# Performance work log

Hardware: AMD Instinct MI355X
Metric: run time of the kernel (lower is better)

## Reference

```python
import jax, jax.numpy as jnp
import numpy as np

B = 48            # graph pairs
NQ, NC = 20, 16   # query / corpus node counts (corpus padded to NMAX)
NMAX = 20         # max_node_set_size
DN, DE = 16, 8    # raw node / edge feature dims
D = 32            # node_state_dim
EH = 64           # edge_hidden_sizes[-1]
EQ, EC = 80, 60   # edges per query / corpus graph
PROP = 5          # n_prop_layers
TEMP = 0.01       # sinkhorn temperature
ITERS = 20        # sinkhorn iterations
LAMBDA = 1.0
NTOT = B * (NQ + NC)
NE = B * (EQ + EC)
SRC, DST = np.triu_indices(NMAX, 1)   # nC2 = 190 node pairs
_indq = np.ones(NMAX, np.int32)
_indc = np.array([1] * NC + [0] * (NMAX - NC), np.int32)
NXOR = jnp.asarray((_indq[:, None] ^ _indc[None, :]).astype(np.float32))  # [20,20]


def _mlp2(x, w1, b1, w2, b2):
    return jnp.maximum(x @ w1 + b1, 0.0) @ w2 + b2


def _sinkhorn(log_alpha):
    la = log_alpha / TEMP
    for _ in range(ITERS):
        la = la - jax.nn.logsumexp(la, axis=2, keepdims=True)
        la = la - jax.nn.logsumexp(la, axis=1, keepdims=True)
    return jnp.exp(la)


def _edge_emb(H, adj, w1, b1, w2, b2):
    s, d = H[:, SRC], H[:, DST]            # [B,nC2,D] gathers
    e = adj[:, SRC, DST][..., None]        # [B,nC2,1]
    f = _mlp2(jnp.concatenate([s, d, e], -1), w1, b1, w2, b2)
    bk = _mlp2(jnp.concatenate([d, s, e], -1), w1, b1, w2, b2)
    return f + bk                          # bidirectional msg, [B,nC2,EH]


def _forward(node_features, edge_features, query_adj, corpus_adj,
             enc_nw, enc_nb, enc_ew, enc_eb,
             msg_w1, msg_b1, msg_w2, msg_b2,
             upd_w1, upd_b1, upd_w2, upd_b2,
             sink_w1, sink_b1, sink_w2, sink_b2,
             lrl_w1, lrl_b1, lrl_w2, lrl_b2,
             from_idx, to_idx):
    h = node_features @ enc_nw + enc_nb    # GMN encoder (linear MLPs)
    e = edge_features @ enc_ew + enc_eb
    for _ in range(PROP):                  # shared-param propagation
        msg = _mlp2(jnp.concatenate([h[from_idx], h[to_idx], e], -1),
                    msg_w1, msg_b1, msg_w2, msg_b2)
        agg = jax.ops.segment_sum(msg, to_idx, num_segments=NTOT)
        h = h + _mlp2(jnp.concatenate([agg, h], -1), upd_w1, upd_b1, upd_w2, upd_b2)
    hp = h.reshape(B, NQ + NC, D)          # split_and_stack (static sizes)
    Hq = hp[:, :NQ]
    Hc = jnp.pad(hp[:, NQ:], ((0, 0), (0, NMAX - NC), (0, 0)))
    tq = _mlp2(Hq, sink_w1, sink_b1, sink_w2, sink_b2)
    tc = _mlp2(Hc, sink_w1, sink_b1, sink_w2, sink_b2)
    cost = jnp.abs(tq[:, :, None, :] - tc[:, None, :, :]).sum(-1)  # cdist p=1
    P = _sinkhorn(-cost)                   # node transport plan [B,20,20]
    Eq = _edge_emb(Hq, query_adj, lrl_w1, lrl_b1, lrl_w2, lrl_b2)
    Ec = _edge_emb(Hc, corpus_adj, lrl_w1, lrl_b1, lrl_w2, lrl_b2)
    Pa, Pb = P[:, SRC, :], P[:, DST, :]
    straight = Pa[:, :, SRC] * Pb[:, :, DST]    # plan[src_i,src_j]*plan[dst_i,dst_j]
    cross = Pa[:, :, DST] * Pb[:, :, SRC]
    eT = straight + cross                  # use_max=False, no second sinkhorn
    aq = query_adj[:, SRC, DST].astype(jnp.int32)
    ac = corpus_adj[:, SRC, DST].astype(jnp.int32)
    pxor = (aq[:, :, None] ^ ac[:, None, :]).astype(P.dtype)
    ediff = Eq[:, :, None, :] - Ec[:, None, :, :]   # [B,nC2,nC2,EH]
    ecost = jnp.maximum(ediff, 0.0).sum(-1) + jnp.maximum(-ediff, 0.0).sum(-1)
    edge_align = (pxor * eT * ecost).sum((-1, -2))
    ndiff = Hq[:, :, None, :] - Hc[:, None, :, :]   # [B,20,20,D]
    ncost = jnp.maximum(ndiff, 0.0).sum(-1) + jnp.maximum(-ndiff, 0.0).sum(-1)
    node_align = (NXOR * P * ncost).sum((-1, -2))
    return edge_align + LAMBDA * node_align         # [B]


def setup_inputs():
    key = jax.random.key(0)
    rng = np.random.default_rng(0)
    base = (np.arange(B) * (NQ + NC))[:, None]
    fq = base + rng.integers(0, NQ, (B, EQ)); tq = base + rng.integers(0, NQ, (B, EQ))
    fc = base + NQ + rng.integers(0, NC, (B, EC)); tc = base + NQ + rng.integers(0, NC, (B, EC))
    from_idx = jnp.asarray(np.concatenate([fq, fc], 1).reshape(-1), jnp.int32)
    to_idx = jnp.asarray(np.concatenate([tq, tc], 1).reshape(-1), jnp.int32)
    qadj = rng.integers(0, 2, (B, NMAX, NMAX)).astype(np.float32)
    cadj = rng.integers(0, 2, (B, NMAX, NMAX)).astype(np.float32)
    cadj[:, NC:, :] = 0.0; cadj[:, :, NC:] = 0.0   # padded corpus nodes have no edges
    ks = iter(jax.random.split(key, 32))
    def w(shape, s=0.1):
        return jax.random.normal(next(ks), shape, jnp.float32) * s
    return {
        'node_features': w((NTOT, DN), 1.0),
        'edge_features': w((NE, DE), 1.0),
        'query_adj': jnp.asarray(qadj),
        'corpus_adj': jnp.asarray(cadj),
        'enc_nw': w((DN, D)), 'enc_nb': w((D,)),
        'enc_ew': w((DE, 16)), 'enc_eb': w((16,)),
        'msg_w1': w((2 * D + 16, EH)), 'msg_b1': w((EH,)),
        'msg_w2': w((EH, EH)), 'msg_b2': w((EH,)),
        'upd_w1': w((EH + D, EH)), 'upd_b1': w((EH,)),
        'upd_w2': w((EH, D)), 'upd_b2': w((D,)),
        'sink_w1': w((D, NMAX)), 'sink_b1': w((NMAX,)),
        'sink_w2': w((NMAX, NMAX)), 'sink_b2': w((NMAX,)),
        'lrl_w1': w((2 * D + 1, EH)), 'lrl_b1': w((EH,)),
        'lrl_w2': w((EH, EH)), 'lrl_b2': w((EH,)),
        'from_idx': from_idx, 'to_idx': to_idx,
        'graph_sizes': jnp.asarray(np.tile([NQ, NC], B), jnp.int32),
    }


def reference(node_features, edge_features, query_adj, corpus_adj,
              enc_nw, enc_nb, enc_ew, enc_eb,
              msg_w1, msg_b1, msg_w2, msg_b2,
              upd_w1, upd_b1, upd_w2, upd_b2,
              sink_w1, sink_b1, sink_w2, sink_b2,
              lrl_w1, lrl_b1, lrl_w2, lrl_b2,
              from_idx, to_idx, graph_sizes):
    return _forward(node_features, edge_features, query_adj, corpus_adj,
                    enc_nw, enc_nb, enc_ew, enc_eb,
                    msg_w1, msg_b1, msg_w2, msg_b2,
                    upd_w1, upd_b1, upd_w2, upd_b2,
                    sink_w1, sink_b1, sink_w2, sink_b2,
                    lrl_w1, lrl_b1, lrl_w2, lrl_b2,
                    from_idx, to_idx)
```

## Files before the change

kernel.cpp:

```cpp
#include <hip/hip_runtime.h>


constexpr int kB    = 48;
constexpr int kNM   = 20;
constexpr int kD    = 32;
constexpr int kNP   = 190;
constexpr int kNTOT = 1728;
constexpr int kIters = 20;
constexpr float kInvT = 100.0f;

__device__ __forceinline__ void pair_sd(int p, int& s, int& d) {
    int row = 0, rem = p;
    #pragma unroll
    for (int r = 0; r < 19; ++r) {
        int len = 19 - r;
        if (rem < len) { row = r; break; }
        rem -= len;
    }
    s = row; d = row + 1 + rem;
}

__device__ __forceinline__ float bc(float v, int k) {
    return __int_as_float(__builtin_amdgcn_readlane(__float_as_int(v), k));
}

__device__ __forceinline__ void lse20(float (&r)[20]) {
    float m01 = fmaxf(r[0], r[1]),  m23 = fmaxf(r[2], r[3]),
          m45 = fmaxf(r[4], r[5]),  m67 = fmaxf(r[6], r[7]),
          m89 = fmaxf(r[8], r[9]),  mab = fmaxf(r[10], r[11]),
          mcd = fmaxf(r[12], r[13]), mef = fmaxf(r[14], r[15]),
          mgh = fmaxf(r[16], r[17]), mij = fmaxf(r[18], r[19]);
    float n0 = fmaxf(m01, m23), n1 = fmaxf(m45, m67), n2 = fmaxf(m89, mab),
          n3 = fmaxf(mcd, mef), n4 = fmaxf(mgh, mij);
    float m = fmaxf(fmaxf(fmaxf(n0, n1), fmaxf(n2, n3)), n4);
    float e[20];
    #pragma unroll
    for (int k = 0; k < 20; ++k) e[k] = __expf(r[k] - m);
    float s01 = e[0] + e[1],  s23 = e[2] + e[3],  s45 = e[4] + e[5],
          s67 = e[6] + e[7],  s89 = e[8] + e[9],  sab = e[10] + e[11],
          scd = e[12] + e[13], sef = e[14] + e[15], sgh = e[16] + e[17],
          sij = e[18] + e[19];
    float t0 = s01 + s23, t1 = s45 + s67, t2 = s89 + sab,
          t3 = scd + sef, t4 = sgh + sij;
    float s = ((t0 + t1) + (t2 + t3)) + t4;
    float l = m + __logf(s);
    #pragma unroll
    for (int k = 0; k < 20; ++k) r[k] -= l;
}

__global__ void k_enc(const float* __restrict__ nf, const float* __restrict__ nw,
                      const float* __restrict__ nb, const float* __restrict__ ef,
                      const float* __restrict__ ew, const float* __restrict__ eb,
                      float* __restrict__ h, float* __restrict__ ee,
                      float* __restrict__ agg, float* __restrict__ out) {
    int tid = blockIdx.x * 256 + threadIdx.x;
    int stride = gridDim.x * 256;
    for (int i = tid; i < kNTOT * 32; i += stride) {
        int n = i >> 5, c = i & 31;
        float acc = nb[c];
        const float* row = nf + n * 16;
        #pragma unroll
        for (int k = 0; k < 16; ++k) acc = fmaf(row[k], nw[k * 32 + c], acc);
        h[i] = acc;
    }
    for (int i = tid; i < 6720 * 16; i += stride) {
        int n = i >> 4, c = i & 15;
        float acc = eb[c];
        const float* row = ef + n * 8;
        #pragma unroll
        for (int k = 0; k < 8; ++k) acc = fmaf(row[k], ew[k * 16 + c], acc);
        ee[i] = acc;
    }
    for (int i = tid; i < kNTOT * 64; i += stride) agg[i] = 0.f;
    if (tid < kB) out[tid] = 0.f;
}

__global__ void __launch_bounds__(256)
k_msg(const float* __restrict__ h, const float* __restrict__ ee,
      const int* __restrict__ fidx, const int* __restrict__ tidx,
      const float* __restrict__ w1, const float* __restrict__ b1,
      const float* __restrict__ w2, const float* __restrict__ b2,
      float* __restrict__ agg) {
    int w = threadIdx.x >> 6, lane = threadIdx.x & 63;
    int e0 = (blockIdx.x * 4 + w) * 2;
    int toj[2]; float xa[2], xb[2], acc[2], o[2];
    #pragma unroll
    for (int j = 0; j < 2; ++j) {
        int e = e0 + j;
        int fr = fidx[e]; toj[j] = tidx[e];
        xa[j] = h[(lane < 32 ? fr : toj[j]) * kD + (lane & 31)];
        xb[j] = ee[e * 16 + (lane & 15)];
        acc[j] = b1[lane];
    }
    #pragma unroll
    for (int k = 0; k < 64; ++k) {
        float w1k = w1[k * 64 + lane];
        #pragma unroll
        for (int j = 0; j < 2; ++j) acc[j] = fmaf(bc(xa[j], k), w1k, acc[j]);
    }
    #pragma unroll
    for (int k = 0; k < 16; ++k) {
        float w1k = w1[(64 + k) * 64 + lane];
        #pragma unroll
        for (int j = 0; j < 2; ++j) acc[j] = fmaf(bc(xb[j], k), w1k, acc[j]);
    }
    #pragma unroll
    for (int j = 0; j < 2; ++j) { acc[j] = fmaxf(acc[j], 0.f); o[j] = b2[lane]; }
    #pragma unroll
    for (int k = 0; k < 64; ++k) {
        float w2k = w2[k * 64 + lane];
        #pragma unroll
        for (int j = 0; j < 2; ++j) o[j] = fmaf(bc(acc[j], k), w2k, o[j]);
    }
    #pragma unroll
    for (int j = 0; j < 2; ++j) atomicAdd(&agg[toj[j] * 64 + lane], o[j]);
}

__global__ void __launch_bounds__(256)
k_upd(float* __restrict__ h, float* __restrict__ agg,
      const float* __restrict__ w1, const float* __restrict__ b1,
      const float* __restrict__ w2, const float* __restrict__ b2) {
    int w = threadIdx.x >> 6, lane = threadIdx.x & 63;
    int n0 = (blockIdx.x * 4 + w) * 2;
    float xa[2], xb[2], acc[2], o[2];
    #pragma unroll
    for (int j = 0; j < 2; ++j) {
        int n = n0 + j;
        xa[j] = agg[n * 64 + lane];
        agg[n * 64 + lane] = 0.f;
        xb[j] = h[n * kD + (lane & 31)];
        acc[j] = b1[lane];
    }
    #pragma unroll
    for (int k = 0; k < 64; ++k) {
        float w1k = w1[k * 64 + lane];
        #pragma unroll
        for (int j = 0; j < 2; ++j) acc[j] = fmaf(bc(xa[j], k), w1k, acc[j]);
    }
    #pragma unroll
    for (int k = 0; k < 32; ++k) {
        float w1k = w1[(64 + k) * 64 + lane];
        #pragma unroll
        for (int j = 0; j < 2; ++j) acc[j] = fmaf(bc(xb[j], k), w1k, acc[j]);
    }
    #pragma unroll
    for (int j = 0; j < 2; ++j) { acc[j] = fmaxf(acc[j], 0.f); o[j] = b2[lane & 31]; }
    #pragma unroll
    for (int k = 0; k < 64; ++k) {
        float w2k = w2[k * 32 + (lane & 31)];
        #pragma unroll
        for (int j = 0; j < 2; ++j) o[j] = fmaf(bc(acc[j], k), w2k, o[j]);
    }
    if (lane < 32) {
        #pragma unroll
        for (int j = 0; j < 2; ++j) h[(n0 + j) * kD + lane] += o[j];
    }
}

__global__ void k_sink_t(const float* __restrict__ h,
                         const float* __restrict__ w1, const float* __restrict__ b1,
                         const float* __restrict__ w2, const float* __restrict__ b2,
                         float* __restrict__ Hq, float* __restrict__ Hc,
                         float* __restrict__ tq, float* __restrict__ tc) {
    __shared__ float xs[4][32];
    __shared__ float hs[4][20];
    int w = threadIdx.x >> 6, lane = threadIdx.x & 63;
    int xcd = blockIdx.x & 7, slot = blockIdx.x >> 3;
    int b = xcd + 8 * (slot / 10);
    int task = (slot % 10) * 4 + w;
    int side = task >= 20;
    int i = task - side * 20;
    if (lane < 32) {
        float v;
        if (side == 0) v = h[(b * 36 + i) * kD + lane];
        else           v = (i < 16) ? h[(b * 36 + 20 + i) * kD + lane] : 0.f;
        (side ? Hc : Hq)[(b * kNM + i) * kD + lane] = v;
        xs[w][lane] = v;
    }
    __syncthreads();
    if (lane < kNM) {
        float acc = b1[lane];
        #pragma unroll
        for (int k = 0; k < kD; ++k) acc += xs[w][k] * w1[k * kNM + lane];
        hs[w][lane] = fmaxf(acc, 0.f);
    }
    __syncthreads();
    if (lane < kNM) {
        float o = b2[lane];
        #pragma unroll
        for (int k = 0; k < kNM; ++k) o += hs[w][k] * w2[k * kNM + lane];
        (side ? tc : tq)[(b * kNM + i) * kNM + lane] = o;
    }
}

__global__ void k_sinkhorn(const float* __restrict__ tq, const float* __restrict__ tc,
                           const float* __restrict__ Hq,
                           float* __restrict__ P, float* __restrict__ out) {
    __shared__ float tcS[400];
    __shared__ float tr[20 * 21];
    int b = blockIdx.x, lane = threadIdx.x;
    for (int i = lane; i < 400; i += 64) tcS[i] = tc[b * 400 + i];
    int i20 = lane < 20 ? lane : 0;
    float tqr[20];
    #pragma unroll
    for (int k = 0; k < 20; ++k) tqr[k] = tq[(b * 20 + i20) * 20 + k];
    __syncthreads();
    float r[20];
    #pragma unroll
    for (int j = 0; j < 20; ++j) {
        float c = 0.f;
        #pragma unroll
        for (int k = 0; k < 20; ++k) c += fabsf(tqr[k] - tcS[j * 20 + k]);
        r[j] = -c * kInvT;
    }
    for (int it = 0; it < kIters; ++it) {
        lse20(r);
        if (lane < 20) {
            #pragma unroll
            for (int j = 0; j < 20; ++j) tr[lane * 21 + j] = r[j];
        }
        __syncthreads();
        if (lane < 20) {
            #pragma unroll
            for (int i = 0; i < 20; ++i) r[i] = tr[i * 21 + lane];
        }
        __syncthreads();
        lse20(r);
        if (lane < 20) {
            #pragma unroll
            for (int i = 0; i < 20; ++i) tr[i * 21 + lane] = r[i];
        }
        __syncthreads();
        if (lane < 20) {
            #pragma unroll
            for (int j = 0; j < 20; ++j) r[j] = tr[lane * 21 + j];
        }
        __syncthreads();
    }
    float part = 0.f;
    if (lane < 20) {
        float pv[20];
        #pragma unroll
        for (int j = 0; j < 20; ++j) pv[j] = __expf(r[j]);
        float* Pb = P + b * 400 + lane * 20;
        #pragma unroll
        for (int j = 0; j < 20; ++j) Pb[j] = pv[j];
        float pr4 = (pv[16] + pv[17]) + (pv[18] + pv[19]);
        float l1 = 0.f;
        const float* hq = Hq + (b * 20 + lane) * 32;
        #pragma unroll
        for (int k = 0; k < 32; ++k) l1 += fabsf(hq[k]);
        part = pr4 * l1;
    }
    #pragma unroll
    for (int off = 32; off; off >>= 1) part += __shfl_down(part, off, 64);
    if (lane == 0) atomicAdd(&out[b], part);
}

__global__ void __launch_bounds__(256)
k_edge_emb(const float* __restrict__ Hq, const float* __restrict__ Hc,
           const float* __restrict__ qadj, const float* __restrict__ cadj,
           const float* __restrict__ w1, const float* __restrict__ b1,
           const float* __restrict__ w2, const float* __restrict__ b2,
           float* __restrict__ Eq, float* __restrict__ Ec) {
    int w = threadIdx.x >> 6, lane = threadIdx.x & 63;
    int xcd = blockIdx.x & 7, slot = blockIdx.x >> 3;
    int b = xcd + 8 * (slot / 24);
    int r = slot % 24;
    float xa[4], ev[4], af[4], ab[4];
    int sidej[4], pj[4];
    #pragma unroll
    for (int j = 0; j < 4; ++j) {
        int tloc = r * 16 + w * 4 + j;
        if (tloc >= 380) tloc = 379;
        sidej[j] = tloc / kNP; pj[j] = tloc % kNP;
        int s, d; pair_sd(pj[j], s, d);
        const float* H = sidej[j] ? Hc : Hq;
        xa[j] = (lane < 32) ? H[(b * kNM + s) * kD + lane]
                            : H[(b * kNM + d) * kD + (lane - 32)];
        ev[j] = (sidej[j] ? cadj : qadj)[b * 400 + s * 20 + d];
        float bb = b1[lane];
        af[j] = bb; ab[j] = bb;
    }
    #pragma unroll
    for (int k = 0; k < 64; ++k) {
        float w1k = w1[k * 64 + lane];
        #pragma unroll
        for (int j = 0; j < 4; ++j) {
            af[j] = fmaf(bc(xa[j], k),      w1k, af[j]);
            ab[j] = fmaf(bc(xa[j], k ^ 32), w1k, ab[j]);
        }
    }
    {
        float w1e = w1[64 * 64 + lane];
        #pragma unroll
        for (int j = 0; j < 4; ++j) {
            af[j] = fmaf(ev[j], w1e, af[j]);
            ab[j] = fmaf(ev[j], w1e, ab[j]);
        }
    }
    float hid[4], o[4];
    #pragma unroll
    for (int j = 0; j < 4; ++j) {
        hid[j] = fmaxf(af[j], 0.f) + fmaxf(ab[j], 0.f);
        o[j] = 2.f * b2[lane];
    }
    #pragma unroll
    for (int k = 0; k < 64; ++k) {
        float w2k = w2[k * 64 + lane];
        #pragma unroll
        for (int j = 0; j < 4; ++j) o[j] = fmaf(bc(hid[j], k), w2k, o[j]);
    }
    #pragma unroll
    for (int j = 0; j < 4; ++j)
        (sidej[j] ? Ec : Eq)[(b * kNP + pj[j]) * 64 + lane] = o[j];
}

#define EC_ALL(X) X(0) X(1) X(2) X(3) X(4) X(5) X(6) X(7) X(8) X(9) X(10) X(11) \
  X(12) X(13) X(14) X(15) X(16) X(17) X(18) X(19) X(20) X(21) X(22) X(23) \
  X(24) X(25) X(26) X(27) X(28) X(29) X(30) X(31)

__global__ void __launch_bounds__(256, 4)
k_final(const float* __restrict__ P, const float* __restrict__ Eq,
        const float* __restrict__ Ec, const float* __restrict__ qadj,
        const float* __restrict__ cadj, float* __restrict__ out) {
    __shared__ float Ps[400];
    __shared__ unsigned char spsh[192], dpsh[192];
    int xcd = blockIdx.x & 7, slot = blockIdx.x >> 3;
    int b = xcd + 8 * (slot / 6), qt = slot % 6;
    int t = threadIdx.x, w = t >> 6, lane = t & 63;
    if (t < 192) {
        int s = 0, d = 0;
        if (t < kNP) pair_sd(t, s, d);
        spsh[t] = (unsigned char)s;
        dpsh[t] = (unsigned char)d;
    }
    for (int i = t; i < 400; i += 256) Ps[i] = P[b * 400 + i];
    __syncthreads();

    int l31 = lane & 31;
    int q = qt * 32 + l31;
    bool qv = q < kNP;
    int sq = spsh[qv ? q : 0], dq = dpsh[qv ? q : 0];
    float acv = qv ? cadj[b * 400 + sq * 20 + dq] : 0.f;

    const float* ecb = Ec + (b * kNP + qt * 32) * 64 + lane;
#define EC_DECL(i) float ec##i = (qt * 32 + i < kNP) ? ecb[i * 64] : 0.f;
    EC_ALL(EC_DECL)
#undef EC_DECL

    float a0 = 0.f, a1 = 0.f, a2 = 0.f, a3 = 0.f;
    int pp = w;
    float aqc = qadj[b * 400 + spsh[pp] * 20 + dpsh[pp]];
    float eqc = Eq[(b * kNP + pp) * 64 + lane];
    while (pp < kNP) {
        int pn = pp + 4;
        float aqn = 0.f, eqn = 0.f;
        if (pn < kNP) {
            aqn = qadj[b * 400 + spsh[pn] * 20 + dpsh[pn]];
            eqn = Eq[(b * kNP + pn) * 64 + lane];
        }
        int sp = spsh[pp], dp = dpsh[pp];
        float eT = Ps[sp * 20 + sq] * Ps[dp * 20 + dq]
                 + Ps[sp * 20 + dq] * Ps[dp * 20 + sq];
        float wqv = qv ? ((aqc > 0.5f) ? (1.f - acv) : acv) * eT : 0.f;
#define EC_FMA(i) { float d_ = fabsf(eqc - ec##i); \
        if ((i & 3) == 0) a0 = fmaf(bc(wqv, i), d_, a0); \
        else if ((i & 3) == 1) a1 = fmaf(bc(wqv, i), d_, a1); \
        else if ((i & 3) == 2) a2 = fmaf(bc(wqv, i), d_, a2); \
        else a3 = fmaf(bc(wqv, i), d_, a3); }
        EC_ALL(EC_FMA)
#undef EC_FMA
        aqc = aqn; eqc = eqn; pp = pn;
    }
    float partial = (a0 + a1) + (a2 + a3);
    #pragma unroll
    for (int off = 32; off; off >>= 1) partial += __shfl_down(partial, off, 64);
    if (lane == 0) atomicAdd(&out[b], partial);
}

extern "C" void kernel_launch(void* const* d_in, const int* in_sizes, int n_in,
                              void* d_out, int out_size, void* d_ws, size_t ws_size,
                              hipStream_t stream) {
    auto f = [&](int i) { return (const float*)d_in[i]; };
    const float* nf   = f(0);
    const float* ef   = f(1);
    const float* qadj = f(2);
    const float* cadj = f(3);
    const int* from_idx = (const int*)d_in[24];
    const int* to_idx   = (const int*)d_in[25];
    float* out = (float*)d_out;

    float* ws  = (float*)d_ws;
    float* h   = ws;
    float* ee  = h   + 55296;
    float* agg = ee  + 107520;
    float* Hq  = agg + 110592;
    float* Hc  = Hq  + 30720;
    float* tq  = Hc  + 30720;
    float* tc  = tq  + 19200;
    float* P   = tc  + 19200;
    float* Eq  = P   + 19200;
    float* Ec  = Eq  + 583680;

    k_enc<<<432, 256, 0, stream>>>(nf, f(4), f(5), ef, f(6), f(7), h, ee, agg, out);
    for (int it = 0; it < 5; ++it) {
        k_msg<<<840, 256, 0, stream>>>(h, ee, from_idx, to_idx,
                                       f(8), f(9), f(10), f(11), agg);
        k_upd<<<216, 256, 0, stream>>>(h, agg, f(12), f(13), f(14), f(15));
    }
    k_sink_t<<<480, 256, 0, stream>>>(h, f(16), f(17), f(18), f(19), Hq, Hc, tq, tc);
    k_sinkhorn<<<48, 64, 0, stream>>>(tq, tc, Hq, P, out);
    k_edge_emb<<<1152, 256, 0, stream>>>(Hq, Hc, qadj, cadj,
                                         f(20), f(21), f(22), f(23), Eq, Ec);
    k_final<<<288, 256, 0, stream>>>(P, Eq, Ec, qadj, cadj, out);
}
```

Baseline: 151.8 us.

## Fuse sinkhorn transform into sinkhorn kernel and restructure final loss with transposed Ec

After: 160.3 us. 1.06x slower.

```diff
diff --git a/kernel.cpp b/kernel.cpp
--- a/kernel.cpp
+++ b/kernel.cpp
@@ -157,104 +157,91 @@
     }
 }
 
-__global__ void k_sink_t(const float* __restrict__ h,
-                         const float* __restrict__ w1, const float* __restrict__ b1,
-                         const float* __restrict__ w2, const float* __restrict__ b2,
-                         float* __restrict__ Hq, float* __restrict__ Hc,
-                         float* __restrict__ tq, float* __restrict__ tc) {
-    __shared__ float xs[4][32];
-    __shared__ float hs[4][20];
-    int w = threadIdx.x >> 6, lane = threadIdx.x & 63;
-    int xcd = blockIdx.x & 7, slot = blockIdx.x >> 3;
-    int b = xcd + 8 * (slot / 10);
-    int task = (slot % 10) * 4 + w;
-    int side = task >= 20;
-    int i = task - side * 20;
-    if (lane < 32) {
-        float v;
-        if (side == 0) v = h[(b * 36 + i) * kD + lane];
-        else           v = (i < 16) ? h[(b * 36 + 20 + i) * kD + lane] : 0.f;
-        (side ? Hc : Hq)[(b * kNM + i) * kD + lane] = v;
-        xs[w][lane] = v;
+__global__ void __launch_bounds__(256)
+k_tail(const float* __restrict__ h,
+       const float* __restrict__ w1, const float* __restrict__ b1,
+       const float* __restrict__ w2, const float* __restrict__ b2,
+       float* __restrict__ Hq, float* __restrict__ Hc,
+       float* __restrict__ P, float* __restrict__ out) {
+    __shared__ float tqS[400], tcS[400];
+    __shared__ float trS[20 * 21];
+    int b = blockIdx.x;
+    int t = threadIdx.x, lane = t & 63, wave = t >> 6;
+
+    for (int task = wave; task < 40; task += 4) {
+        int side = task >= 20, i = task - side * 20;
+        float v = 0.f;
+        if (lane < 32) {
+            if (!side)        v = h[(b * 36 + i) * kD + lane];
+            else if (i < 16)  v = h[(b * 36 + 20 + i) * kD + lane];
+            (side ? Hc : Hq)[(b * kNM + i) * kD + lane] = v;
+        }
+        int tt = lane < 20 ? lane : 0;
+        float acc = b1[tt];
+        #pragma unroll
+        for (int k = 0; k < 32; ++k) acc = fmaf(bc(v, k), w1[k * 20 + tt], acc);
+        acc = fmaxf(acc, 0.f);
+        float o = b2[tt];
+        #pragma unroll
+        for (int k = 0; k < 20; ++k) o = fmaf(bc(acc, k), w2[k * 20 + tt], o);
+        if (lane < 20) (side ? tcS : tqS)[i * 20 + lane] = o;
     }
     __syncthreads();
-    if (lane < kNM) {
-        float acc = b1[lane];
-        #pragma unroll
-        for (int k = 0; k < kD; ++k) acc += xs[w][k] * w1[k * kNM + lane];
-        hs[w][lane] = fmaxf(acc, 0.f);
-    }
-    __syncthreads();
-    if (lane < kNM) {
-        float o = b2[lane];
-        #pragma unroll
-        for (int k = 0; k < kNM; ++k) o += hs[w][k] * w2[k * kNM + lane];
-        (side ? tc : tq)[(b * kNM + i) * kNM + lane] = o;
-    }
-}
-
-__global__ void k_sinkhorn(const float* __restrict__ tq, const float* __restrict__ tc,
-                           const float* __restrict__ Hq,
-                           float* __restrict__ P, float* __restrict__ out) {
-    __shared__ float tcS[400];
-    __shared__ float tr[20 * 21];
-    int b = blockIdx.x, lane = threadIdx.x;
-    for (int i = lane; i < 400; i += 64) tcS[i] = tc[b * 400 + i];
-    int i20 = lane < 20 ? lane : 0;
-    float tqr[20];
-    #pragma unroll
-    for (int k = 0; k < 20; ++k) tqr[k] = tq[(b * 20 + i20) * 20 + k];
-    __syncthreads();
+
     float r[20];
-    #pragma unroll
-    for (int j = 0; j < 20; ++j) {
-        float c = 0.f;
-        #pragma unroll
-        for (int k = 0; k < 20; ++k) c += fabsf(tqr[k] - tcS[j * 20 + k]);
-        r[j] = -c * kInvT;
+    if (t < 20) {
+        float tqr[20];
+        #pragma unroll
+        for (int k = 0; k < 20; ++k) tqr[k] = tqS[t * 20 + k];
+        #pragma unroll
+        for (int j = 0; j < 20; ++j) {
+            float c = 0.f;
+            #pragma unroll
+            for (int k = 0; k < 20; ++k) c += fabsf(tqr[k] - tcS[j * 20 + k]);
+            r[j] = -c * kInvT;
+        }
     }
     for (int it = 0; it < kIters; ++it) {
-        lse20(r);
-        if (lane < 20) {
+        if (t < 20) {
+            lse20(r);
             #pragma unroll
-            for (int j = 0; j < 20; ++j) tr[lane * 21 + j] = r[j];
+            for (int j = 0; j < 20; ++j) trS[t * 21 + j] = r[j];
         }
         __syncthreads();
-        if (lane < 20) {
+        if (t < 20) {
             #pragma unroll
-            for (int i = 0; i < 20; ++i) r[i] = tr[i * 21 + lane];
+            for (int i = 0; i < 20; ++i) r[i] = trS[i * 21 + t];
+            lse20(r);
+            #pragma unroll
+            for (int i = 0; i < 20; ++i) trS[i * 21 + t] = r[i];
         }
         __syncthreads();
-        lse20(r);
-        if (lane < 20) {
+        if (t < 20) {
             #pragma unroll
-            for (int i = 0; i < 20; ++i) tr[i * 21 + lane] = r[i];
+            for (int j = 0; j < 20; ++j) r[j] = trS[t * 21 + j];
         }
         __syncthreads();
-        if (lane < 20) {
-            #pragma unroll
-            for (int j = 0; j < 20; ++j) r[j] = tr[lane * 21 + j];
-        }
-        __syncthreads();
     }
     float part = 0.f;
-    if (lane < 20) {
+    if (t < 20) {
         float pv[20];
         #pragma unroll
         for (int j = 0; j < 20; ++j) pv[j] = __expf(r[j]);
-        float* Pb = P + b * 400 + lane * 20;
+        float* Pb = P + b * 400 + t * 20;
         #pragma unroll
         for (int j = 0; j < 20; ++j) Pb[j] = pv[j];
         float pr4 = (pv[16] + pv[17]) + (pv[18] + pv[19]);
         float l1 = 0.f;
-        const float* hq = Hq + (b * 20 + lane) * 32;
+        const float* hq = h + (b * 36 + t) * kD;
         #pragma unroll
         for (int k = 0; k < 32; ++k) l1 += fabsf(hq[k]);
         part = pr4 * l1;
     }
-    #pragma unroll
-    for (int off = 32; off; off >>= 1) part += __shfl_down(part, off, 64);
-    if (lane == 0) atomicAdd(&out[b], part);
+    if (t < 64) {
+        #pragma unroll
+        for (int off = 32; off; off >>= 1) part += __shfl_down(part, off, 64);
+        if (t == 0) atomicAdd(&out[b], part);
+    }
 }
 
 __global__ void __launch_bounds__(256)
@@ -262,7 +249,7 @@
            const float* __restrict__ qadj, const float* __restrict__ cadj,
            const float* __restrict__ w1, const float* __restrict__ b1,
            const float* __restrict__ w2, const float* __restrict__ b2,
-           float* __restrict__ Eq, float* __restrict__ Ec) {
+           float* __restrict__ Eq, float* __restrict__ EcT) {
     int w = threadIdx.x >> 6, lane = threadIdx.x & 63;
     int xcd = blockIdx.x & 7, slot = blockIdx.x >> 3;
     int b = xcd + 8 * (slot / 24);
@@ -312,22 +299,29 @@
         for (int j = 0; j < 4; ++j) o[j] = fmaf(bc(hid[j], k), w2k, o[j]);
     }
     #pragma unroll
-    for (int j = 0; j < 4; ++j)
-        (sidej[j] ? Ec : Eq)[(b * kNP + pj[j]) * 64 + lane] = o[j];
-}
-
-#define EC_ALL(X) X(0) X(1) X(2) X(3) X(4) X(5) X(6) X(7) X(8) X(9) X(10) X(11) \
+    for (int j = 0; j < 4; ++j) {
+        if (sidej[j]) EcT[(b * 64 + lane) * kNP + pj[j]] = o[j];
+        else          Eq[(b * kNP + pj[j]) * 64 + lane] = o[j];
+    }
+}
+
+#define EC64(X) X(0) X(1) X(2) X(3) X(4) X(5) X(6) X(7) X(8) X(9) X(10) X(11) \
   X(12) X(13) X(14) X(15) X(16) X(17) X(18) X(19) X(20) X(21) X(22) X(23) \
-  X(24) X(25) X(26) X(27) X(28) X(29) X(30) X(31)
-
-__global__ void __launch_bounds__(256, 4)
+  X(24) X(25) X(26) X(27) X(28) X(29) X(30) X(31) X(32) X(33) X(34) X(35) \
+  X(36) X(37) X(38) X(39) X(40) X(41) X(42) X(43) X(44) X(45) X(46) X(47) \
+  X(48) X(49) X(50) X(51) X(52) X(53) X(54) X(55) X(56) X(57) X(58) X(59) \
+  X(60) X(61) X(62) X(63)
+
+__global__ void __launch_bounds__(256)
 k_final(const float* __restrict__ P, const float* __restrict__ Eq,
-        const float* __restrict__ Ec, const float* __restrict__ qadj,
+        const float* __restrict__ EcT, const float* __restrict__ qadj,
         const float* __restrict__ cadj, float* __restrict__ out) {
     __shared__ float Ps[400];
     __shared__ unsigned char spsh[192], dpsh[192];
     int xcd = blockIdx.x & 7, slot = blockIdx.x >> 3;
-    int b = xcd + 8 * (slot / 6), qt = slot % 6;
+    int b = xcd + 8 * (slot / 6);
+    int r = slot % 6;
+    int qt = r >> 1, ph = r & 1;
     int t = threadIdx.x, w = t >> 6, lane = t & 63;
     if (t < 192) {
         int s = 0, d = 0;
@@ -338,45 +332,40 @@
     for (int i = t; i < 400; i += 256) Ps[i] = P[b * 400 + i];
     __syncthreads();
 
-    int l31 = lane & 31;
-    int q = qt * 32 + l31;
+    int q = qt * 64 + lane;
     bool qv = q < kNP;
-    int sq = spsh[qv ? q : 0], dq = dpsh[qv ? q : 0];
+    int qc = qv ? q : 0;
+    int sq = spsh[qc], dq = dpsh[qc];
     float acv = qv ? cadj[b * 400 + sq * 20 + dq] : 0.f;
 
-    const float* ecb = Ec + (b * kNP + qt * 32) * 64 + lane;
-#define EC_DECL(i) float ec##i = (qt * 32 + i < kNP) ? ecb[i * 64] : 0.f;
-    EC_ALL(EC_DECL)
-#undef EC_DECL
-
-    float a0 = 0.f, a1 = 0.f, a2 = 0.f, a3 = 0.f;
-    int pp = w;
-    float aqc = qadj[b * 400 + spsh[pp] * 20 + dpsh[pp]];
-    float eqc = Eq[(b * kNP + pp) * 64 + lane];
-    while (pp < kNP) {
-        int pn = pp + 4;
-        float aqn = 0.f, eqn = 0.f;
-        if (pn < kNP) {
-            aqn = qadj[b * 400 + spsh[pn] * 20 + dpsh[pn]];
-            eqn = Eq[(b * kNP + pn) * 64 + lane];
-        }
-        int sp = spsh[pp], dp = dpsh[pp];
+    const float* ecb = EcT + b * 64 * kNP + qc;
+#define ECD(i) float ec##i = ecb[(i) * kNP];
+    EC64(ECD)
+#undef ECD
+
+    float acc = 0.f;
+    for (int p = ph * 4 + w; p < kNP; p += 8) {
+        int sp = spsh[p], dp = dpsh[p];
+        float aq = qadj[b * 400 + sp * 20 + dp];
+        const float4* eqr = (const float4*)(Eq + (b * kNP + p) * 64);
+        float ce0 = 0.f, ce1 = 0.f;
+#define QS(k, i0, i1, i2, i3) { float4 e = eqr[k]; \
+        ce0 += fabsf(e.x - ec##i0) + fabsf(e.y - ec##i1); \
+        ce1 += fabsf(e.z - ec##i2) + fabsf(e.w - ec##i3); }
+        QS(0,0,1,2,3)     QS(1,4,5,6,7)     QS(2,8,9,10,11)    QS(3,12,13,14,15)
+        QS(4,16,17,18,19) QS(5,20,21,22,23) QS(6,24,25,26,27)  QS(7,28,29,30,31)
+        QS(8,32,33,34,35) QS(9,36,37,38,39) QS(10,40,41,42,43) QS(11,44,45,46,47)
+        QS(12,48,49,50,51) QS(13,52,53,54,55) QS(14,56,57,58,59) QS(15,60,61,62,63)
+#undef QS
         float eT = Ps[sp * 20 + sq] * Ps[dp * 20 + dq]
                  + Ps[sp * 20 + dq] * Ps[dp * 20 + sq];
-        float wqv = qv ? ((aqc > 0.5f) ? (1.f - acv) : acv) * eT : 0.f;
-#define EC_FMA(i) { float d_ = fabsf(eqc - ec##i); \
-        if ((i & 3) == 0) a0 = fmaf(bc(wqv, i), d_, a0); \
-        else if ((i & 3) == 1) a1 = fmaf(bc(wqv, i), d_, a1); \
-        else if ((i & 3) == 2) a2 = fmaf(bc(wqv, i), d_, a2); \
-        else a3 = fmaf(bc(wqv, i), d_, a3); }
-        EC_ALL(EC_FMA)
-#undef EC_FMA
-        aqc = aqn; eqc = eqn; pp = pn;
-    }
-    float partial = (a0 + a1) + (a2 + a3);
-    #pragma unroll
-    for (int off = 32; off; off >>= 1) partial += __shfl_down(partial, off, 64);
-    if (lane == 0) atomicAdd(&out[b], partial);
+        float gate = (aq > 0.5f) ? (1.f - acv) : acv;
+        float wq = qv ? gate * eT : 0.f;
+        acc = fmaf(wq, ce0 + ce1, acc);
+    }
+    #pragma unroll
+    for (int off = 32; off; off >>= 1) acc += __shfl_down(acc, off, 64);
+    if (lane == 0) atomicAdd(&out[b], acc);
 }
 
 extern "C" void kernel_launch(void* const* d_in, const int* in_sizes, int n_in,
@@ -397,11 +386,9 @@
     float* agg = ee  + 107520;
     float* Hq  = agg + 110592;
     float* Hc  = Hq  + 30720;
-    float* tq  = Hc  + 30720;
-    float* tc  = tq  + 19200;
-    float* P   = tc  + 19200;
+    float* P   = Hc  + 30720;
     float* Eq  = P   + 19200;
-    float* Ec  = Eq  + 583680;
+    float* EcT = Eq  + 583680;
 
     k_enc<<<432, 256, 0, stream>>>(nf, f(4), f(5), ef, f(6), f(7), h, ee, agg, out);
     for (int it = 0; it < 5; ++it) {
@@ -409,9 +396,8 @@
                                        f(8), f(9), f(10), f(11), agg);
         k_upd<<<216, 256, 0, stream>>>(h, agg, f(12), f(13), f(14), f(15));
     }
-    k_sink_t<<<480, 256, 0, stream>>>(h, f(16), f(17), f(18), f(19), Hq, Hc, tq, tc);
-    k_sinkhorn<<<48, 64, 0, stream>>>(tq, tc, Hq, P, out);
+    k_tail<<<48, 256, 0, stream>>>(h, f(16), f(17), f(18), f(19), Hq, Hc, P, out);
     k_edge_emb<<<1152, 256, 0, stream>>>(Hq, Hc, qadj, cadj,
-                                         f(20), f(21), f(22), f(23), Eq, Ec);
-    k_final<<<288, 256, 0, stream>>>(P, Eq, Ec, qadj, cadj, out);
-}
+                                         f(20), f(21), f(22), f(23), Eq, EcT);
+    k_final<<<288, 256, 0, stream>>>(P, Eq, EcT, qadj, cadj, out);
+}
```
